# Performance work log

Measured on AMD Instinct MI355X. Metric: run time of the kernel, lower is better.

The kernel has to match this reference:

```python
import jax, jax.numpy as jnp
import numpy as np

B, H, W = 512, 30, 30
NUM_COLORS, IN_DIM, HID, OUT_DIM, NUM_LAYERS = 10, 12, 128, 64, 4
LN_EPS = 1e-5


def _grid_edge_index(h, w):
    # 4-connectivity, both directions, plus self-loops (PyG GCNConv default add_self_loops=True)
    idx = np.arange(h * w).reshape(h, w)
    src = np.concatenate([idx[:, :-1].ravel(), idx[:, 1:].ravel(),
                          idx[:-1, :].ravel(), idx[1:, :].ravel(), idx.ravel()])
    dst = np.concatenate([idx[:, 1:].ravel(), idx[:, :-1].ravel(),
                          idx[1:, :].ravel(), idx[:-1, :].ravel(), idx.ravel()])
    return np.stack([src, dst]).astype(np.int32)


def setup_inputs() -> dict:
    key = jax.random.key(0)
    ks = jax.random.split(key, 10)
    p = lambda k, shape: (jax.random.normal(k, shape, dtype=jnp.float32) * 0.02)
    grids = jax.random.randint(ks[0], (B, H, W), 0, NUM_COLORS, dtype=jnp.int32)
    return {
        "grids": grids,
        "edge_index": jnp.asarray(_grid_edge_index(H, W)),
        "Win": p(ks[1], (IN_DIM, HID)),
        "bin_": jnp.zeros((HID,), jnp.float32),
        "Wg": p(ks[2], (NUM_LAYERS, HID, HID)),
        "bg": jnp.zeros((NUM_LAYERS, HID), jnp.float32),
        "gamma": jnp.ones((NUM_LAYERS, HID), jnp.float32),
        "beta": jnp.zeros((NUM_LAYERS, HID), jnp.float32),
        "Wout": p(ks[3], (HID, OUT_DIM)),
        "bout": jnp.zeros((OUT_DIM,), jnp.float32),
    }


def _layer_norm(x, g, b):
    m = jnp.mean(x, axis=-1, keepdims=True)
    v = jnp.var(x, axis=-1, keepdims=True)
    return (x - m) * jax.lax.rsqrt(v + LN_EPS) * g + b


def reference(grids, edge_index, Win, bin_, Wg, bg, gamma, beta, Wout, bout):
    Bb, Hh, Ww = grids.shape
    N = Hh * Ww
    src, dst = edge_index[0], edge_index[1]

    # symmetric GCN normalization: D^{-1/2} (A+I) D^{-1/2}
    deg = jax.ops.segment_sum(jnp.ones_like(dst, jnp.float32), dst, num_segments=N)
    dinv = jax.lax.rsqrt(jnp.maximum(deg, 1.0))
    coef = (dinv[src] * dinv[dst])[:, None]  # [E,1]

    # node features: one-hot color + normalized (row, col) positions
    rows = jnp.repeat(jnp.arange(Hh, dtype=jnp.float32) / max(Hh - 1, 1), Ww)
    cols = jnp.tile(jnp.arange(Ww, dtype=jnp.float32) / max(Ww - 1, 1), Hh)
    pos = jnp.stack([rows, cols], axis=-1)  # [N,2]

    def encode(grid_flat):  # grid_flat: [N] int
        feat = jnp.concatenate([jax.nn.one_hot(grid_flat, NUM_COLORS, dtype=jnp.float32), pos], axis=-1)
        x = jax.nn.relu(feat @ Win + bin_)  # [N,HID]
        for i in range(NUM_LAYERS):
            h = x @ Wg[i]
            agg = jax.ops.segment_sum(h[src] * coef, dst, num_segments=N) + bg[i]
            x = jax.nn.relu(_layer_norm(agg, gamma[i], beta[i])) + x
        return x @ Wout + bout  # [N,OUT_DIM]

    return jax.vmap(encode)(grids.reshape(Bb, N))
```

## Files before the change

### kernel.cpp

```cpp
#include <hip/hip_runtime.h>

#define HID 128
#define ODIM 64

typedef _Float16 half8 __attribute__((ext_vector_type(8)));
typedef float f32x4 __attribute__((ext_vector_type(4)));

typedef const __attribute__((address_space(1))) void* as1cvp;
typedef __attribute__((address_space(3))) void* as3vp;

__device__ __forceinline__ void gload16(const void* g, void* l) {
  __builtin_amdgcn_global_load_lds((as1cvp)g, (as3vp)l, 16, 0, 0);
}

__global__ __launch_bounds__(256) void k_prep(
    const float* __restrict__ Wg, const float* __restrict__ Wout,
    _Float16* __restrict__ WspHi, _Float16* __restrict__ WspLo,
    _Float16* __restrict__ WhHi, _Float16* __restrict__ WhLo) {
  int i = blockIdx.x * 256 + threadIdx.x;
  if (i < 65536) {
    int j = i & 7, n = (i >> 3) & 127, g = (i >> 10) & 3, kc = (i >> 12) & 3, l = i >> 14;
    int k = kc * 32 + g * 8 + j;
    float v = Wg[(size_t)(l * 128 + k) * 128 + n];
    WspHi[i] = (_Float16)v;
  } else if (i < 131072) {
    int m = i - 65536;
    int j = m & 7, n = (m >> 3) & 127, g = (m >> 10) & 3, kc = (m >> 12) & 3, l = m >> 14;
    int k = kc * 32 + g * 8 + j;
    float v = Wg[(size_t)(l * 128 + k) * 128 + n];
    _Float16 h = (_Float16)v;
    WspLo[m] = (_Float16)(v - (float)h);
  } else if (i < 139264) {
    int m = i - 131072;
    int j = m & 7, n = (m >> 3) & 63, g = (m >> 9) & 3, kc = m >> 11;
    int k = kc * 32 + g * 8 + j;
    float v = Wout[k * 64 + n];
    WhHi[m] = (_Float16)v;
  } else if (i < 147456) {
    int m = i - 139264;
    int j = m & 7, n = (m >> 3) & 63, g = (m >> 9) & 3, kc = m >> 11;
    int k = kc * 32 + g * 8 + j;
    float v = Wout[k * 64 + n];
    _Float16 h = (_Float16)v;
    WhLo[m] = (_Float16)(v - (float)h);
  }
}

__global__ __launch_bounds__(256) void k_encode(
    const int* __restrict__ grids, const float* __restrict__ Win,
    const float* __restrict__ binp, float* __restrict__ X, int b0, int nodes) {
  int t = blockIdx.x * 256 + threadIdx.x;
  if (t >= nodes * 32) return;
  int node = t >> 5;
  int i = t & 31;
  int n = node % 900;
  int b = node / 900;
  int r = n / 30, c = n - r * 30;
  int color = grids[(b0 + b) * 900 + n];
  float fr = (float)r / 29.0f, fc = (float)c / 29.0f;
  f32x4 wc = ((const f32x4*)(Win + color * HID))[i];
  f32x4 wr = ((const f32x4*)(Win + 10 * HID))[i];
  f32x4 wl = ((const f32x4*)(Win + 11 * HID))[i];
  f32x4 bb = ((const f32x4*)binp)[i];
  f32x4 v = wc + fr * wr + fc * wl + bb;
#pragma unroll
  for (int j = 0; j < 4; ++j) v[j] = fmaxf(v[j], 0.0f);
  ((f32x4*)(X + (size_t)node * HID))[i] = v;
}

__global__ __launch_bounds__(512, 4) void k_hidden(
    const float* __restrict__ Xin, float* __restrict__ Xout,
    const _Float16* __restrict__ Whi, const _Float16* __restrict__ Wlo,
    const float* __restrict__ bgp, const float* __restrict__ gamp,
    const float* __restrict__ betp, int nodesTotal) {
  __shared__ __attribute__((aligned(16))) float Xt[2][192 * 32];
  __shared__ __attribute__((aligned(16))) _Float16 WTh[2][4 * 128 * 8];
  __shared__ __attribute__((aligned(16))) _Float16 WTl[2][4 * 128 * 8];

  const int t = threadIdx.x;
  const int lane = t & 63;
  const int wave = t >> 6;
  const int q = lane >> 4, l16 = lane & 15;

  int nwg = gridDim.x, bid = blockIdx.x;
  int qd = nwg >> 3, rm = nwg & 7;
  int xcd = bid & 7, idx = bid >> 3;
  int wg = (xcd < rm ? xcd * (qd + 1) : rm * (qd + 1) + (xcd - rm) * qd) + idx;
  const int blockRow0 = wg * 128;
  const int waveRow0 = blockRow0 + wave * 16;

  int off[5];
  float wts[5];
  {
    int nd = waveRow0 + l16;
    if (nd > nodesTotal - 1) nd = nodesTotal - 1;
    int n = nd % 900;
    int r = n / 30, c = n - r * 30;
    int loc = nd - blockRow0 + 30;
    int nb[5] = {loc, loc - 30, loc + 30, loc - 1, loc + 1};
    float dc = rsqrtf((float)(1 + (r > 0) + (r < 29) + (c > 0) + (c < 29)));
    wts[0] = dc * dc;
    wts[1] = (r > 0) ? dc * rsqrtf((float)(2 + (r > 1) + (c > 0) + (c < 29))) : 0.f;
    wts[2] = (r < 29) ? dc * rsqrtf((float)(2 + (r < 28) + (c > 0) + (c < 29))) : 0.f;
    wts[3] = (c > 0) ? dc * rsqrtf((float)(2 + (r > 0) + (r < 29) + (c > 1))) : 0.f;
    wts[4] = (c < 29) ? dc * rsqrtf((float)(2 + (r > 0) + (r < 29) + (c < 28))) : 0.f;
#pragma unroll
    for (int e = 0; e < 5; ++e)
      off[e] = nb[e] * 32 + (((2 * q) ^ (nb[e] & 7)) << 2);
  }

  auto stage = [&](int kc, int buf) {
#pragma unroll
    for (int s = 0; s < 3; ++s) {
      int f = t + s * 512;
      int row = f >> 3, v = f & 7;
      int gr = blockRow0 - 30 + row;
      gr = gr < 0 ? 0 : (gr > nodesTotal - 1 ? nodesTotal - 1 : gr);
      gload16(Xin + (size_t)gr * HID + kc * 32 + ((v ^ (row & 7)) << 2),
              &Xt[buf][(s * 512 + wave * 64) * 4]);
    }
    gload16(Whi + kc * 4096 + t * 8, &WTh[buf][wave * 64 * 8]);
    gload16(Wlo + kc * 4096 + t * 8, &WTl[buf][wave * 64 * 8]);
  };

  f32x4 acc[8];
#pragma unroll
  for (int nt = 0; nt < 8; ++nt) acc[nt] = (f32x4){0.f, 0.f, 0.f, 0.f};

  stage(0, 0);
  __syncthreads();

  for (int kc = 0; kc < 4; ++kc) {
    const int cur = kc & 1;
    if (kc < 3) stage(kc + 1, cur ^ 1);

    half8 Ahi, Alo;
    {
      const float* Xb = Xt[cur];
      f32x4 s0 = {0.f, 0.f, 0.f, 0.f}, s1 = {0.f, 0.f, 0.f, 0.f};
#pragma unroll
      for (int e = 0; e < 5; ++e) {
        s0 += wts[e] * (*(const f32x4*)(Xb + off[e]));
        s1 += wts[e] * (*(const f32x4*)(Xb + (off[e] ^ 4)));
      }
#pragma unroll
      for (int j = 0; j < 4; ++j) {
        _Float16 h0 = (_Float16)s0[j];
        Ahi[j] = h0;
        Alo[j] = (_Float16)(s0[j] - (float)h0);
        _Float16 h1 = (_Float16)s1[j];
        Ahi[4 + j] = h1;
        Alo[4 + j] = (_Float16)(s1[j] - (float)h1);
      }
    }
#pragma unroll
    for (int nt = 0; nt < 8; ++nt) {
      int n = nt * 16 + l16;
      half8 bhi = *(const half8*)(&WTh[cur][(q * 128 + n) * 8]);
      half8 blo = *(const half8*)(&WTl[cur][(q * 128 + n) * 8]);
      acc[nt] = __builtin_amdgcn_mfma_f32_16x16x32_f16(Alo, bhi, acc[nt], 0, 0, 0);
      acc[nt] = __builtin_amdgcn_mfma_f32_16x16x32_f16(Ahi, blo, acc[nt], 0, 0, 0);
      acc[nt] = __builtin_amdgcn_mfma_f32_16x16x32_f16(Ahi, bhi, acc[nt], 0, 0, 0);
    }
    if (kc < 3) __syncthreads();
  }

  float bgv[8], gv[8], btv[8];
#pragma unroll
  for (int nt = 0; nt < 8; ++nt) {
    int cl = nt * 16 + l16;
    bgv[nt] = bgp[cl];
    gv[nt] = gamp[cl];
    btv[nt] = betp[cl];
  }
#pragma unroll
  for (int reg = 0; reg < 4; ++reg) {
    float rs = 0.f;
#pragma unroll
    for (int nt = 0; nt < 8; ++nt) {
      acc[nt][reg] += bgv[nt];
      rs += acc[nt][reg];
    }
    rs += __shfl_xor(rs, 1, 64);
    rs += __shfl_xor(rs, 2, 64);
    rs += __shfl_xor(rs, 4, 64);
    rs += __shfl_xor(rs, 8, 64);
    float mean = rs * (1.f / 128.f);
    float ss = 0.f;
#pragma unroll
    for (int nt = 0; nt < 8; ++nt) {
      float d = acc[nt][reg] - mean;
      ss += d * d;
    }
    ss += __shfl_xor(ss, 1, 64);
    ss += __shfl_xor(ss, 2, 64);
    ss += __shfl_xor(ss, 4, 64);
    ss += __shfl_xor(ss, 8, 64);
    float rsd = rsqrtf(ss * (1.f / 128.f) + 1e-5f);
    int row = waveRow0 + q * 4 + reg;
    if (row < nodesTotal) {
      const float* xr = Xin + (size_t)row * HID;
      float* xo = Xout + (size_t)row * HID;
#pragma unroll
      for (int nt = 0; nt < 8; ++nt) {
        int col = nt * 16 + l16;
        float y = fmaxf((acc[nt][reg] - mean) * rsd * gv[nt] + btv[nt], 0.f);
        xo[col] = y + xr[col];
      }
    }
  }
}

__global__ __launch_bounds__(512, 4) void k_hidden3(
    const float* __restrict__ Xin, float* __restrict__ Outp,
    const _Float16* __restrict__ Whi, const _Float16* __restrict__ Wlo,
    const float* __restrict__ bgp, const float* __restrict__ gamp,
    const float* __restrict__ betp, const _Float16* __restrict__ WhHig,
    const _Float16* __restrict__ WhLog, const float* __restrict__ boutp,
    int nodesTotal) {
  __shared__ __attribute__((aligned(16))) char smem[81920];
  float* XtB = (float*)smem;
  _Float16* WThB = (_Float16*)(smem + 49152);
  _Float16* WTlB = (_Float16*)(smem + 65536);

  const int t = threadIdx.x;
  const int lane = t & 63;
  const int wave = t >> 6;
  const int q = lane >> 4, l16 = lane & 15;

  int nwg = gridDim.x, bid = blockIdx.x;
  int qd = nwg >> 3, rm = nwg & 7;
  int xcd = bid & 7, idx = bid >> 3;
  int wg = (xcd < rm ? xcd * (qd + 1) : rm * (qd + 1) + (xcd - rm) * qd) + idx;
  const int blockRow0 = wg * 128;
  const int waveRow0 = blockRow0 + wave * 16;

  int off[5];
  float wts[5];
  {
    int nd = waveRow0 + l16;
    if (nd > nodesTotal - 1) nd = nodesTotal - 1;
    int n = nd % 900;
    int r = n / 30, c = n - r * 30;
    int loc = nd - blockRow0 + 30;
    int nb[5] = {loc, loc - 30, loc + 30, loc - 1, loc + 1};
    float dc = rsqrtf((float)(1 + (r > 0) + (r < 29) + (c > 0) + (c < 29)));
    wts[0] = dc * dc;
    wts[1] = (r > 0) ? dc * rsqrtf((float)(2 + (r > 1) + (c > 0) + (c < 29))) : 0.f;
    wts[2] = (r < 29) ? dc * rsqrtf((float)(2 + (r < 28) + (c > 0) + (c < 29))) : 0.f;
    wts[3] = (c > 0) ? dc * rsqrtf((float)(2 + (r > 0) + (r < 29) + (c > 1))) : 0.f;
    wts[4] = (c < 29) ? dc * rsqrtf((float)(2 + (r > 0) + (r < 29) + (c < 28))) : 0.f;
#pragma unroll
    for (int e = 0; e < 5; ++e)
      off[e] = nb[e] * 32 + (((2 * q) ^ (nb[e] & 7)) << 2);
  }

  auto stage = [&](int kc, int buf) {
#pragma unroll
    for (int s = 0; s < 3; ++s) {
      int f = t + s * 512;
      int row = f >> 3, v = f & 7;
      int gr = blockRow0 - 30 + row;
      gr = gr < 0 ? 0 : (gr > nodesTotal - 1 ? nodesTotal - 1 : gr);
      gload16(Xin + (size_t)gr * HID + kc * 32 + ((v ^ (row & 7)) << 2),
              XtB + buf * 6144 + (s * 512 + wave * 64) * 4);
    }
    gload16(Whi + kc * 4096 + t * 8, WThB + buf * 4096 + wave * 512);
    gload16(Wlo + kc * 4096 + t * 8, WTlB + buf * 4096 + wave * 512);
  };

  f32x4 acc[8];
#pragma unroll
  for (int nt = 0; nt < 8; ++nt) acc[nt] = (f32x4){0.f, 0.f, 0.f, 0.f};

  stage(0, 0);
  __syncthreads();

  for (int kc = 0; kc < 4; ++kc) {
    const int cur = kc & 1;
    if (kc < 3) stage(kc + 1, cur ^ 1);

    half8 Ahi, Alo;
    {
      const float* Xb = XtB + cur * 6144;
      f32x4 s0 = {0.f, 0.f, 0.f, 0.f}, s1 = {0.f, 0.f, 0.f, 0.f};
#pragma unroll
      for (int e = 0; e < 5; ++e) {
        s0 += wts[e] * (*(const f32x4*)(Xb + off[e]));
        s1 += wts[e] * (*(const f32x4*)(Xb + (off[e] ^ 4)));
      }
#pragma unroll
      for (int j = 0; j < 4; ++j) {
        _Float16 h0 = (_Float16)s0[j];
        Ahi[j] = h0;
        Alo[j] = (_Float16)(s0[j] - (float)h0);
        _Float16 h1 = (_Float16)s1[j];
        Ahi[4 + j] = h1;
        Alo[4 + j] = (_Float16)(s1[j] - (float)h1);
      }
    }
#pragma unroll
    for (int nt = 0; nt < 8; ++nt) {
      int n = nt * 16 + l16;
      half8 bhi = *(const half8*)(WThB + cur * 4096 + (q * 128 + n) * 8);
      half8 blo = *(const half8*)(WTlB + cur * 4096 + (q * 128 + n) * 8);
      acc[nt] = __builtin_amdgcn_mfma_f32_16x16x32_f16(Alo, bhi, acc[nt], 0, 0, 0);
      acc[nt] = __builtin_amdgcn_mfma_f32_16x16x32_f16(Ahi, blo, acc[nt], 0, 0, 0);
      acc[nt] = __builtin_amdgcn_mfma_f32_16x16x32_f16(Ahi, bhi, acc[nt], 0, 0, 0);
    }
    __syncthreads();
  }

  _Float16* Xhi = (_Float16*)smem;
  _Float16* Xlo = (_Float16*)(smem + 32768);
  float bgv[8], gv[8], btv[8];
#pragma unroll
  for (int nt = 0; nt < 8; ++nt) {
    int cl = nt * 16 + l16;
    bgv[nt] = bgp[cl];
    gv[nt] = gamp[cl];
    btv[nt] = betp[cl];
  }
#pragma unroll
  for (int reg = 0; reg < 4; ++reg) {
    float rs = 0.f;
#pragma unroll
    for (int nt = 0; nt < 8; ++nt) {
      acc[nt][reg] += bgv[nt];
      rs += acc[nt][reg];
    }
    rs += __shfl_xor(rs, 1, 64);
    rs += __shfl_xor(rs, 2, 64);
    rs += __shfl_xor(rs, 4, 64);
    rs += __shfl_xor(rs, 8, 64);
    float mean = rs * (1.f / 128.f);
    float ss = 0.f;
#pragma unroll
    for (int nt = 0; nt < 8; ++nt) {
      float d = acc[nt][reg] - mean;
      ss += d * d;
    }
    ss += __shfl_xor(ss, 1, 64);
    ss += __shfl_xor(ss, 2, 64);
    ss += __shfl_xor(ss, 4, 64);
    ss += __shfl_xor(ss, 8, 64);
    float rsd = rsqrtf(ss * (1.f / 128.f) + 1e-5f);
    int row = waveRow0 + q * 4 + reg;
    int lr = wave * 16 + q * 4 + reg;
    if (row < nodesTotal) {
      const float* xr = Xin + (size_t)row * HID;
#pragma unroll
      for (int nt = 0; nt < 8; ++nt) {
        int col = nt * 16 + l16;
        float y = fmaxf((acc[nt][reg] - mean) * rsd * gv[nt] + btv[nt], 0.f);
        float fx = y + xr[col];
        int sg = (col >> 3) ^ (lr & 7);
        int pa = lr * 128 + sg * 8 + (col & 7);
        _Float16 h = (_Float16)fx;
        Xhi[pa] = h;
        Xlo[pa] = (_Float16)(fx - (float)h);
      }
    }
  }
  __syncthreads();

  f32x4 hacc[4];
#pragma unroll
  for (int nt = 0; nt < 4; ++nt) hacc[nt] = (f32x4){0.f, 0.f, 0.f, 0.f};
  const int alr = wave * 16 + l16;
#pragma unroll
  for (int kc = 0; kc < 4; ++kc) {
    int ag = (kc * 4 + q) ^ (alr & 7);
    half8 ahi = *(const half8*)(Xhi + alr * 128 + ag * 8);
    half8 alo = *(const half8*)(Xlo + alr * 128 + ag * 8);
#pragma unroll
    for (int nt = 0; nt < 4; ++nt) {
      int n = nt * 16 + l16;
      half8 bhi = *(const half8*)(WhHig + kc * 2048 + q * 512 + n * 8);
      half8 blo = *(const half8*)(WhLog + kc * 2048 + q * 512 + n * 8);
      hacc[nt] = __builtin_amdgcn_mfma_f32_16x16x32_f16(alo, bhi, hacc[nt], 0, 0, 0);
      hacc[nt] = __builtin_amdgcn_mfma_f32_16x16x32_f16(ahi, blo, hacc[nt], 0, 0, 0);
      hacc[nt] = __builtin_amdgcn_mfma_f32_16x16x32_f16(ahi, bhi, hacc[nt], 0, 0, 0);
    }
  }
  float bv[4];
#pragma unroll
  for (int nt = 0; nt < 4; ++nt) bv[nt] = boutp[nt * 16 + l16];
#pragma unroll
  for (int reg = 0; reg < 4; ++reg) {
    int row = waveRow0 + q * 4 + reg;
    if (row < nodesTotal) {
      float* op = Outp + (size_t)row * ODIM;
#pragma unroll
      for (int nt = 0; nt < 4; ++nt)
        op[nt * 16 + l16] = hacc[nt][reg] + bv[nt];
    }
  }
}

extern "C" void kernel_launch(void* const* d_in, const int* in_sizes, int n_in,
                              void* d_out, int out_size, void* d_ws, size_t ws_size,
                              hipStream_t stream) {
  const int* grids = (const int*)d_in[0];
  const float* Win  = (const float*)d_in[2];
  const float* bin  = (const float*)d_in[3];
  const float* Wg   = (const float*)d_in[4];
  const float* bg   = (const float*)d_in[5];
  const float* gam  = (const float*)d_in[6];
  const float* bet  = (const float*)d_in[7];
  const float* Wout = (const float*)d_in[8];
  const float* bout = (const float*)d_in[9];
  float* Out = (float*)d_out;

  _Float16* WspHi = (_Float16*)d_ws;
  _Float16* WspLo = WspHi + 65536;
  _Float16* WhHi  = WspHi + 131072;
  _Float16* WhLo  = WspHi + 139264;
  const size_t wBytes = 294912;

  const int Btot = 512;
  const size_t perBatchBytes = (size_t)900 * HID * 4 * 2;
  size_t xws = ws_size > wBytes ? ws_size - wBytes : 0;
  int chunkB = (int)(xws / perBatchBytes);
  if (chunkB > Btot) chunkB = Btot;
  if (chunkB < 1) chunkB = 1;
  int nch = (Btot + chunkB - 1) / chunkB;

  float* Xa = (float*)((char*)d_ws + wBytes);
  float* Xb = Xa + (size_t)chunkB * 900 * HID;

  k_prep<<<dim3(576), dim3(256), 0, stream>>>(Wg, Wout, WspHi, WspLo, WhHi, WhLo);

  for (int ci = 0; ci < nch; ++ci) {
    int b0 = ci * chunkB;
    int cb = Btot - b0;
    if (cb > chunkB) cb = chunkB;
    int nodes = cb * 900;
    int gbh = (nodes + 127) / 128;

    k_encode<<<dim3((nodes * 32 + 255) / 256), dim3(256), 0, stream>>>(
        grids, Win, bin, Xa, b0, nodes);
    float* src = Xa;
    float* dst = Xb;
    for (int l = 0; l < 3; ++l) {
      k_hidden<<<dim3(gbh), dim3(512), 0, stream>>>(
          src, dst, WspHi + l * 16384, WspLo + l * 16384,
          bg + l * HID, gam + l * HID, bet + l * HID, nodes);
      float* tmp = src; src = dst; dst = tmp;
    }
    k_hidden3<<<dim3(gbh), dim3(512), 0, stream>>>(
        src, Out + (size_t)b0 * 900 * ODIM, WspHi + 3 * 16384, WspLo + 3 * 16384,
        bg + 3 * HID, gam + 3 * HID, bet + 3 * HID, WhHi, WhLo, bout, nodes);
  }
}
```

Before: 825.5 us.

## Store activations in K-chunk planar layout and fuse weight prep into encode

The node-feature buffers change from row-major [node][128] to four planes of [node][32], one per 32-wide K chunk, so each staged chunk load reads a contiguous block rather than 128-byte pieces strided by 512 bytes. The epilogue reads and writes use the same planar indexing. The separate weight-conversion kernel is merged into the encode kernel as extra blocks on the first chunk, removing one launch. The planar layout may make the epilogue stores less contiguous per row, and the merged prep blocks run alongside encode blocks.

```diff
diff --git a/kernel.cpp b/kernel.cpp
--- a/kernel.cpp
+++ b/kernel.cpp
@@ -13,42 +13,44 @@
   __builtin_amdgcn_global_load_lds((as1cvp)g, (as3vp)l, 16, 0, 0);
 }
 
-__global__ __launch_bounds__(256) void k_prep(
-    const float* __restrict__ Wg, const float* __restrict__ Wout,
-    _Float16* __restrict__ WspHi, _Float16* __restrict__ WspLo,
-    _Float16* __restrict__ WhHi, _Float16* __restrict__ WhLo) {
-  int i = blockIdx.x * 256 + threadIdx.x;
-  if (i < 65536) {
-    int j = i & 7, n = (i >> 3) & 127, g = (i >> 10) & 3, kc = (i >> 12) & 3, l = i >> 14;
-    int k = kc * 32 + g * 8 + j;
-    float v = Wg[(size_t)(l * 128 + k) * 128 + n];
-    WspHi[i] = (_Float16)v;
-  } else if (i < 131072) {
-    int m = i - 65536;
-    int j = m & 7, n = (m >> 3) & 127, g = (m >> 10) & 3, kc = (m >> 12) & 3, l = m >> 14;
-    int k = kc * 32 + g * 8 + j;
-    float v = Wg[(size_t)(l * 128 + k) * 128 + n];
-    _Float16 h = (_Float16)v;
-    WspLo[m] = (_Float16)(v - (float)h);
-  } else if (i < 139264) {
-    int m = i - 131072;
-    int j = m & 7, n = (m >> 3) & 63, g = (m >> 9) & 3, kc = m >> 11;
-    int k = kc * 32 + g * 8 + j;
-    float v = Wout[k * 64 + n];
-    WhHi[m] = (_Float16)v;
-  } else if (i < 147456) {
-    int m = i - 139264;
-    int j = m & 7, n = (m >> 3) & 63, g = (m >> 9) & 3, kc = m >> 11;
-    int k = kc * 32 + g * 8 + j;
-    float v = Wout[k * 64 + n];
-    _Float16 h = (_Float16)v;
-    WhLo[m] = (_Float16)(v - (float)h);
-  }
-}
-
-__global__ __launch_bounds__(256) void k_encode(
+
+__global__ __launch_bounds__(256) void k_encode_prep(
     const int* __restrict__ grids, const float* __restrict__ Win,
-    const float* __restrict__ binp, float* __restrict__ X, int b0, int nodes) {
+    const float* __restrict__ binp, float* __restrict__ X, int b0, int nodes,
+    int PS, int gbe, const float* __restrict__ Wg,
+    const float* __restrict__ Wout, _Float16* __restrict__ WspHi,
+    _Float16* __restrict__ WspLo, _Float16* __restrict__ WhHi,
+    _Float16* __restrict__ WhLo) {
+  if (blockIdx.x >= gbe) {
+    int i = (blockIdx.x - gbe) * 256 + threadIdx.x;
+    if (i < 65536) {
+      int j = i & 7, n = (i >> 3) & 127, g = (i >> 10) & 3, kc = (i >> 12) & 3, l = i >> 14;
+      int k = kc * 32 + g * 8 + j;
+      float v = Wg[(size_t)(l * 128 + k) * 128 + n];
+      WspHi[i] = (_Float16)v;
+    } else if (i < 131072) {
+      int m = i - 65536;
+      int j = m & 7, n = (m >> 3) & 127, g = (m >> 10) & 3, kc = (m >> 12) & 3, l = m >> 14;
+      int k = kc * 32 + g * 8 + j;
+      float v = Wg[(size_t)(l * 128 + k) * 128 + n];
+      _Float16 h = (_Float16)v;
+      WspLo[m] = (_Float16)(v - (float)h);
+    } else if (i < 139264) {
+      int m = i - 131072;
+      int j = m & 7, n = (m >> 3) & 63, g = (m >> 9) & 3, kc = m >> 11;
+      int k = kc * 32 + g * 8 + j;
+      float v = Wout[k * 64 + n];
+      WhHi[m] = (_Float16)v;
+    } else if (i < 147456) {
+      int m = i - 139264;
+      int j = m & 7, n = (m >> 3) & 63, g = (m >> 9) & 3, kc = m >> 11;
+      int k = kc * 32 + g * 8 + j;
+      float v = Wout[k * 64 + n];
+      _Float16 h = (_Float16)v;
+      WhLo[m] = (_Float16)(v - (float)h);
+    }
+    return;
+  }
   int t = blockIdx.x * 256 + threadIdx.x;
   if (t >= nodes * 32) return;
   int node = t >> 5;
@@ -65,14 +67,14 @@
   f32x4 v = wc + fr * wr + fc * wl + bb;
 #pragma unroll
   for (int j = 0; j < 4; ++j) v[j] = fmaxf(v[j], 0.0f);
-  ((f32x4*)(X + (size_t)node * HID))[i] = v;
+  *(f32x4*)(X + (size_t)(i >> 3) * PS + (size_t)node * 32 + (i & 7) * 4) = v;
 }
 
 __global__ __launch_bounds__(512, 4) void k_hidden(
     const float* __restrict__ Xin, float* __restrict__ Xout,
     const _Float16* __restrict__ Whi, const _Float16* __restrict__ Wlo,
     const float* __restrict__ bgp, const float* __restrict__ gamp,
-    const float* __restrict__ betp, int nodesTotal) {
+    const float* __restrict__ betp, int nodesTotal, int PS) {
   __shared__ __attribute__((aligned(16))) float Xt[2][192 * 32];
   __shared__ __attribute__((aligned(16))) _Float16 WTh[2][4 * 128 * 8];
   __shared__ __attribute__((aligned(16))) _Float16 WTl[2][4 * 128 * 8];
@@ -110,13 +112,14 @@
   }
 
   auto stage = [&](int kc, int buf) {
+    const float* Xp = Xin + (size_t)kc * PS;
 #pragma unroll
     for (int s = 0; s < 3; ++s) {
       int f = t + s * 512;
       int row = f >> 3, v = f & 7;
       int gr = blockRow0 - 30 + row;
       gr = gr < 0 ? 0 : (gr > nodesTotal - 1 ? nodesTotal - 1 : gr);
-      gload16(Xin + (size_t)gr * HID + kc * 32 + ((v ^ (row & 7)) << 2),
+      gload16(Xp + (size_t)gr * 32 + ((v ^ (row & 7)) << 2),
               &Xt[buf][(s * 512 + wave * 64) * 4]);
     }
     gload16(Whi + kc * 4096 + t * 8, &WTh[buf][wave * 64 * 8]);
@@ -199,13 +202,11 @@
     float rsd = rsqrtf(ss * (1.f / 128.f) + 1e-5f);
     int row = waveRow0 + q * 4 + reg;
     if (row < nodesTotal) {
-      const float* xr = Xin + (size_t)row * HID;
-      float* xo = Xout + (size_t)row * HID;
 #pragma unroll
       for (int nt = 0; nt < 8; ++nt) {
-        int col = nt * 16 + l16;
+        size_t pofs = (size_t)(nt >> 1) * PS + (size_t)row * 32 + (nt & 1) * 16 + l16;
         float y = fmaxf((acc[nt][reg] - mean) * rsd * gv[nt] + btv[nt], 0.f);
-        xo[col] = y + xr[col];
+        Xout[pofs] = y + Xin[pofs];
       }
     }
   }
@@ -217,7 +218,7 @@
     const float* __restrict__ bgp, const float* __restrict__ gamp,
     const float* __restrict__ betp, const _Float16* __restrict__ WhHig,
     const _Float16* __restrict__ WhLog, const float* __restrict__ boutp,
-    int nodesTotal) {
+    int nodesTotal, int PS) {
   __shared__ __attribute__((aligned(16))) char smem[81920];
   float* XtB = (float*)smem;
   _Float16* WThB = (_Float16*)(smem + 49152);
@@ -256,13 +257,14 @@
   }
 
   auto stage = [&](int kc, int buf) {
+    const float* Xp = Xin + (size_t)kc * PS;
 #pragma unroll
     for (int s = 0; s < 3; ++s) {
       int f = t + s * 512;
       int row = f >> 3, v = f & 7;
       int gr = blockRow0 - 30 + row;
       gr = gr < 0 ? 0 : (gr > nodesTotal - 1 ? nodesTotal - 1 : gr);
-      gload16(Xin + (size_t)gr * HID + kc * 32 + ((v ^ (row & 7)) << 2),
+      gload16(Xp + (size_t)gr * 32 + ((v ^ (row & 7)) << 2),
               XtB + buf * 6144 + (s * 512 + wave * 64) * 4);
     }
     gload16(Whi + kc * 4096 + t * 8, WThB + buf * 4096 + wave * 512);
@@ -348,12 +350,12 @@
     int row = waveRow0 + q * 4 + reg;
     int lr = wave * 16 + q * 4 + reg;
     if (row < nodesTotal) {
-      const float* xr = Xin + (size_t)row * HID;
 #pragma unroll
       for (int nt = 0; nt < 8; ++nt) {
         int col = nt * 16 + l16;
+        size_t pofs = (size_t)(nt >> 1) * PS + (size_t)row * 32 + (nt & 1) * 16 + l16;
         float y = fmaxf((acc[nt][reg] - mean) * rsd * gv[nt] + btv[nt], 0.f);
-        float fx = y + xr[col];
+        float fx = y + Xin[pofs];
         int sg = (col >> 3) ^ (lr & 7);
         int pa = lr * 128 + sg * 8 + (col & 7);
         _Float16 h = (_Float16)fx;
@@ -426,10 +428,9 @@
   if (chunkB < 1) chunkB = 1;
   int nch = (Btot + chunkB - 1) / chunkB;
 
+  const int PS = chunkB * 900 * 32;
   float* Xa = (float*)((char*)d_ws + wBytes);
-  float* Xb = Xa + (size_t)chunkB * 900 * HID;
-
-  k_prep<<<dim3(576), dim3(256), 0, stream>>>(Wg, Wout, WspHi, WspLo, WhHi, WhLo);
+  float* Xb = Xa + (size_t)PS * 4;
 
   for (int ci = 0; ci < nch; ++ci) {
     int b0 = ci * chunkB;
@@ -438,18 +439,21 @@
     int nodes = cb * 900;
     int gbh = (nodes + 127) / 128;
 
-    k_encode<<<dim3((nodes * 32 + 255) / 256), dim3(256), 0, stream>>>(
-        grids, Win, bin, Xa, b0, nodes);
+    int gbe = (nodes * 32 + 255) / 256;
+    int gtot = gbe + (ci == 0 ? 576 : 0);
+    k_encode_prep<<<dim3(gtot), dim3(256), 0, stream>>>(
+        grids, Win, bin, Xa, b0, nodes, PS, gbe, Wg, Wout,
+        WspHi, WspLo, WhHi, WhLo);
     float* src = Xa;
     float* dst = Xb;
     for (int l = 0; l < 3; ++l) {
       k_hidden<<<dim3(gbh), dim3(512), 0, stream>>>(
           src, dst, WspHi + l * 16384, WspLo + l * 16384,
-          bg + l * HID, gam + l * HID, bet + l * HID, nodes);
+          bg + l * HID, gam + l * HID, bet + l * HID, nodes, PS);
       float* tmp = src; src = dst; dst = tmp;
     }
     k_hidden3<<<dim3(gbh), dim3(512), 0, stream>>>(
         src, Out + (size_t)b0 * 900 * ODIM, WspHi + 3 * 16384, WspLo + 3 * 16384,
-        bg + 3 * HID, gam + 3 * HID, bet + 3 * HID, WhHi, WhLo, bout, nodes);
+        bg + 3 * HID, gam + 3 * HID, bet + 3 * HID, WhHi, WhLo, bout, nodes, PS);
   }
 }
```

After: 804.4 us. 1.03x faster.
